# Optimization experiments

Hardware: AMD Instinct MI355X
Metric: run time of the kernel (lower is better)

Reference implementation:

```python
import jax, jax.numpy as jnp
import numpy as np

H = 16  # n_heads

def setup_inputs() -> dict:
    key = jax.random.key(0)
    ks = jax.random.split(key, 7)
    B, L, D = 4, 2048, 1024
    s = 0.02
    return {
        "z": jax.random.normal(ks[0], (B, L, D), jnp.float32),
        "connection": jax.random.normal(ks[1], (B, L, D), jnp.float32),
        "Wq": jax.random.normal(ks[2], (2 * D, D), jnp.float32) * s,
        "Wk": jax.random.normal(ks[3], (2 * D, D), jnp.float32) * s,
        "Wv": jax.random.normal(ks[4], (D, D), jnp.float32) * s,
        "Wo": jax.random.normal(ks[5], (D, D), jnp.float32) * s,
        "temp": jnp.float32(1.0),
    }

def reference(z, connection, Wq, Wk, Wv, Wo, temp):
    B, L, D = z.shape
    hd = D // H
    zc = jnp.concatenate([z, connection], axis=-1)          # [B,L,2D]
    Q = (zc @ Wq).reshape(B, L, H, hd).transpose(0, 2, 1, 3)  # [B,H,L,hd]
    K = (zc @ Wk).reshape(B, L, H, hd).transpose(0, 2, 1, 3)
    V = (z @ Wv).reshape(B, L, H, hd).transpose(0, 2, 1, 3)
    scale = (hd ** -0.5) * temp
    scores = jnp.einsum('bhqd,bhkd->bhqk', Q, K) * scale     # [B,H,L,L]
    rel = jax.nn.sigmoid(scores)
    rel_sum = jnp.clip(rel.sum(-1, keepdims=True), 1.0, None)
    out = jnp.einsum('bhqk,bhkd->bhqd', rel, V) / rel_sum
    out = out.transpose(0, 2, 1, 3).reshape(B, L, D)
    return out @ Wo
```

## Files before the change

kernel.cpp:

```cpp
#include <hip/hip_runtime.h>

typedef unsigned short u16;
typedef unsigned int u32;
typedef __bf16 bf16x8 __attribute__((ext_vector_type(8)));
typedef float f32x4 __attribute__((ext_vector_type(4)));

#define DEV static __device__ __forceinline__

DEV void gload16(const void* g, void* l) {
    __builtin_amdgcn_global_load_lds(
        (const __attribute__((address_space(1))) void*)g,
        (__attribute__((address_space(3))) void*)l, 16, 0, 0);
}

DEV void store_c(float* p, float v) { *p = v; }
DEV void store_c(u16* p, float v) { *(__bf16*)p = (__bf16)v; }

DEV int swz(int row, int bytecol) { return row * 128 + (bytecol ^ ((row & 7) << 4)); }
DEV int swzP(int row, int bytecol) {
    return row * 128 + (bytecol ^ ((row & 7) << 4) ^ (row & 8));
}

DEV void xcd_remap(int& bx, int& by, int gx, int gy) {
    int nwg = gx * gy;
    int bid = by * gx + bx;
    int logical = (bid & 7) * (nwg >> 3) + (bid >> 3);
    bx = logical % gx;
    by = logical / gx;
}

__global__ void pack_zc(const float* __restrict__ z, const float* __restrict__ cn,
                        u16* __restrict__ zc) {
    size_t i = ((size_t)blockIdx.x * blockDim.x + threadIdx.x) * 4;
    size_t t = i >> 11;
    int c = (int)(i & 2047);
    const float* src = (c < 1024) ? (z + t * 1024 + c) : (cn + t * 1024 + (c - 1024));
    float4 v = *reinterpret_cast<const float4*>(src);
    union { __bf16 h[4]; uint2 u; } o;
    o.h[0] = (__bf16)v.x; o.h[1] = (__bf16)v.y;
    o.h[2] = (__bf16)v.z; o.h[3] = (__bf16)v.w;
    *reinterpret_cast<uint2*>(zc + i) = o.u;
}

__global__ void transpose_conv_w(const float* __restrict__ W, u16* __restrict__ WT,
                                 int K, int N, const float* __restrict__ scl) {
    __shared__ float tile[32][33];
    float sc = scl ? scl[0] * 0.18033688011112042f : 1.0f;
    int n0 = blockIdx.x * 32, k0 = blockIdx.y * 32;
    int tx = threadIdx.x, ty = threadIdx.y;
    #pragma unroll
    for (int i = ty; i < 32; i += 8)
        tile[i][tx] = W[(size_t)(k0 + i) * N + n0 + tx];
    __syncthreads();
    #pragma unroll
    for (int i = ty; i < 32; i += 8)
        *(__bf16*)&WT[(size_t)(n0 + i) * K + k0 + tx] = (__bf16)(tile[tx][i] * sc);
}

__global__ void transpose_v(const u16* __restrict__ Vf, u16* __restrict__ Vt) {
    __shared__ u16 tile[32][33];
    int bh = blockIdx.z; int b = bh >> 4, h = bh & 15;
    int l0 = blockIdx.x * 32, d0 = blockIdx.y * 32;
    int tx = threadIdx.x, ty = threadIdx.y;
    #pragma unroll
    for (int i = ty; i < 32; i += 8)
        tile[i][tx] = Vf[(size_t)(b * 2048 + l0 + i) * 1024 + h * 64 + d0 + tx];
    __syncthreads();
    #pragma unroll
    for (int i = ty; i < 32; i += 8)
        Vt[((size_t)bh * 64 + d0 + i) * 2048 + l0 + tx] = tile[tx][i];
}

template <typename OutT>
__global__ __launch_bounds__(256, 2)
void gemm_bt(const u16* __restrict__ A, const u16* __restrict__ BT,
             OutT* __restrict__ C, int M, int N, int K,
             int lda, int ldb, int ldc) {
    __shared__ u16 As[128 * 64];
    __shared__ u16 Bs[128 * 64];
    const int tid = threadIdx.x;
    const int lane = tid & 63;
    const int wid = tid >> 6;
    int bx = blockIdx.x, by = blockIdx.y;
    xcd_remap(bx, by, gridDim.x, gridDim.y);
    const int m0 = bx * 128;
    const int n0 = by * 128;
    const int wr = (wid >> 1) * 64;
    const int wc = (wid & 1) * 64;

    f32x4 acc[4][4];
    #pragma unroll
    for (int i = 0; i < 4; ++i)
        #pragma unroll
        for (int j = 0; j < 4; ++j)
            acc[i][j] = f32x4{0.f, 0.f, 0.f, 0.f};

    const int srcoff = ((lane & 7) ^ (lane >> 3)) * 8;
    const int rb = wid * 32 + (lane >> 3);
    const u16* aptr[4]; const u16* bptr[4];
    #pragma unroll
    for (int p = 0; p < 4; ++p) {
        aptr[p] = A  + (size_t)(m0 + rb + p * 8) * lda + srcoff;
        bptr[p] = BT + (size_t)(n0 + rb + p * 8) * ldb + srcoff;
    }

    for (int k0 = 0; k0 < K; k0 += 64) {
        __syncthreads();
        #pragma unroll
        for (int p = 0; p < 4; ++p)
            gload16(aptr[p] + k0, (char*)As + (wid * 4 + p) * 1024);
        #pragma unroll
        for (int p = 0; p < 4; ++p)
            gload16(bptr[p] + k0, (char*)Bs + (wid * 4 + p) * 1024);
        __syncthreads();

        #pragma unroll
        for (int kk = 0; kk < 64; kk += 32) {
            bf16x8 af[4], bfr[4];
            #pragma unroll
            for (int i = 0; i < 4; ++i) {
                int row = wr + i * 16 + (lane & 15);
                af[i] = *reinterpret_cast<const bf16x8*>(
                    reinterpret_cast<const char*>(As) + swz(row, (kk + (lane >> 4) * 8) * 2));
            }
            #pragma unroll
            for (int j = 0; j < 4; ++j) {
                int row = wc + j * 16 + (lane & 15);
                bfr[j] = *reinterpret_cast<const bf16x8*>(
                    reinterpret_cast<const char*>(Bs) + swz(row, (kk + (lane >> 4) * 8) * 2));
            }
            #pragma unroll
            for (int i = 0; i < 4; ++i)
                #pragma unroll
                for (int j = 0; j < 4; ++j)
                    acc[i][j] = __builtin_amdgcn_mfma_f32_16x16x32_bf16(af[i], bfr[j], acc[i][j], 0, 0, 0);
        }
    }

    #pragma unroll
    for (int i = 0; i < 4; ++i)
        #pragma unroll
        for (int j = 0; j < 4; ++j)
            #pragma unroll
            for (int r = 0; r < 4; ++r) {
                int row = m0 + wr + i * 16 + (lane >> 4) * 4 + r;
                int col = n0 + wc + j * 16 + (lane & 15);
                store_c(&C[(size_t)row * ldc + col], acc[i][j][r]);
            }
}

__global__ __launch_bounds__(256, 2)
void attn_kernel(const u16* __restrict__ QKf, const u16* __restrict__ Vt,
                 u16* __restrict__ Oa) {
    constexpr int L = 2048, D = 1024, QKLD = 2048, HD = 64;
    __shared__ u16 Ks[2][64 * 64];
    __shared__ u16 Vs[2][64 * 64];
    __shared__ u16 Ps[4][32 * 64];

    const int tid = threadIdx.x;
    const int lane = tid & 63;
    const int wid = tid >> 6;
    const int hi = lane >> 4;
    const int lq = lane & 15;
    int bx = blockIdx.x, by = blockIdx.y;
    xcd_remap(bx, by, gridDim.x, gridDim.y);
    const int bh = by;
    const int b = bh >> 4, h = bh & 15;
    const int q0 = bx * 128;

    const u16* Qbase = QKf + (size_t)(b * L) * QKLD + h * HD;
    const u16* Kbase = Qbase + 1024;
    const u16* Vbase = Vt + (size_t)bh * HD * L;

    const int srcoff = ((lane & 7) ^ (lane >> 3)) * 8;
    const int rb = wid * 16 + (lane >> 3);
    const u16* kptr[2]; const u16* vptr[2];
    #pragma unroll
    for (int p = 0; p < 2; ++p) {
        kptr[p] = Kbase + (size_t)(rb + p * 8) * QKLD + srcoff;
        vptr[p] = Vbase + (size_t)(rb + p * 8) * L + srcoff;
    }

    bf16x8 qf[2][2];
    #pragma unroll
    for (int i = 0; i < 2; ++i)
        #pragma unroll
        for (int kx = 0; kx < 2; ++kx)
            qf[i][kx] = *reinterpret_cast<const bf16x8*>(
                Qbase + (size_t)(q0 + wid * 32 + i * 16 + lq) * QKLD + kx * 32 + hi * 8);

    #pragma unroll
    for (int p = 0; p < 2; ++p)
        gload16(kptr[p], (char*)Ks[0] + (wid * 2 + p) * 1024);
    #pragma unroll
    for (int p = 0; p < 2; ++p)
        gload16(vptr[p], (char*)Vs[0] + (wid * 2 + p) * 1024);

    bf16x8 onesf;
    #pragma unroll
    for (int j = 0; j < 8; ++j) onesf[j] = (__bf16)1.0f;

    f32x4 oacc[4][2];
    #pragma unroll
    for (int ct = 0; ct < 4; ++ct)
        #pragma unroll
        for (int i = 0; i < 2; ++i) oacc[ct][i] = f32x4{0.f, 0.f, 0.f, 0.f};
    f32x4 racc[2];
    racc[0] = f32x4{0.f, 0.f, 0.f, 0.f};
    racc[1] = f32x4{0.f, 0.f, 0.f, 0.f};

    __syncthreads();
    int cur = 0;

    for (int k0 = 0; k0 < L; k0 += 64) {
        if (k0 + 64 < L) {
            #pragma unroll
            for (int p = 0; p < 2; ++p)
                gload16(kptr[p] + (size_t)(k0 + 64) * QKLD, (char*)Ks[cur ^ 1] + (wid * 2 + p) * 1024);
            #pragma unroll
            for (int p = 0; p < 2; ++p)
                gload16(vptr[p] + (k0 + 64), (char*)Vs[cur ^ 1] + (wid * 2 + p) * 1024);
        }

        f32x4 s[4][2];
        #pragma unroll
        for (int ct = 0; ct < 4; ++ct)
            #pragma unroll
            for (int i = 0; i < 2; ++i) s[ct][i] = f32x4{0.f, 0.f, 0.f, 0.f};
        #pragma unroll
        for (int kx = 0; kx < 2; ++kx) {
            bf16x8 ak[4];
            #pragma unroll
            for (int ct = 0; ct < 4; ++ct) {
                int krow = ct * 16 + lq;
                ak[ct] = *reinterpret_cast<const bf16x8*>(
                    reinterpret_cast<const char*>(Ks[cur]) + swz(krow, kx * 64 + hi * 16));
            }
            #pragma unroll
            for (int ct = 0; ct < 4; ++ct)
                #pragma unroll
                for (int i = 0; i < 2; ++i)
                    s[ct][i] = __builtin_amdgcn_mfma_f32_16x16x32_bf16(ak[ct], qf[i][kx], s[ct][i], 0, 0, 0);
        }

        #pragma unroll
        for (int i = 0; i < 2; ++i) {
            int prow = i * 16 + lq;
            #pragma unroll
            for (int ct = 0; ct < 4; ++ct) {
                float t0 = 1.0f + __builtin_amdgcn_exp2f(-s[ct][i][0]);
                float t1 = 1.0f + __builtin_amdgcn_exp2f(-s[ct][i][1]);
                float t2 = 1.0f + __builtin_amdgcn_exp2f(-s[ct][i][2]);
                float t3 = 1.0f + __builtin_amdgcn_exp2f(-s[ct][i][3]);
                float m01 = t0 * t1, m23 = t2 * t3;
                float rall = __builtin_amdgcn_rcpf(m01 * m23);
                float r01 = m23 * rall, r23 = m01 * rall;
                union { __bf16 hh[4]; uint2 uu; } pk;
                pk.hh[0] = (__bf16)(t1 * r01);
                pk.hh[1] = (__bf16)(t0 * r01);
                pk.hh[2] = (__bf16)(t3 * r23);
                pk.hh[3] = (__bf16)(t2 * r23);
                *reinterpret_cast<uint2*>(reinterpret_cast<char*>(Ps[wid]) +
                    swzP(prow, ct * 32 + hi * 8)) = pk.uu;
            }
        }

        #pragma unroll
        for (int kx = 0; kx < 2; ++kx) {
            bf16x8 ap[2];
            #pragma unroll
            for (int i = 0; i < 2; ++i) {
                int prow = i * 16 + lq;
                union { u32 w[4]; bf16x8 v; } apu;
                *reinterpret_cast<uint2*>(&apu.w[0]) = *reinterpret_cast<const uint2*>(
                    reinterpret_cast<const char*>(Ps[wid]) + swzP(prow, kx * 64 + hi * 16));
                *reinterpret_cast<uint2*>(&apu.w[2]) = *reinterpret_cast<const uint2*>(
                    reinterpret_cast<const char*>(Ps[wid]) + swzP(prow, kx * 64 + hi * 16 + 8));
                ap[i] = apu.v;
            }
            racc[0] = __builtin_amdgcn_mfma_f32_16x16x32_bf16(ap[0], onesf, racc[0], 0, 0, 0);
            racc[1] = __builtin_amdgcn_mfma_f32_16x16x32_bf16(ap[1], onesf, racc[1], 0, 0, 0);
            #pragma unroll
            for (int ct = 0; ct < 4; ++ct) {
                int vrow = ct * 16 + lq;
                bf16x8 bv = *reinterpret_cast<const bf16x8*>(
                    reinterpret_cast<const char*>(Vs[cur]) + swz(vrow, kx * 64 + hi * 16));
                #pragma unroll
                for (int i = 0; i < 2; ++i)
                    oacc[ct][i] = __builtin_amdgcn_mfma_f32_16x16x32_bf16(ap[i], bv, oacc[ct][i], 0, 0, 0);
            }
        }

        __syncthreads();
        cur ^= 1;
    }

    float rdiv[2][4];
    #pragma unroll
    for (int i = 0; i < 2; ++i)
        #pragma unroll
        for (int r = 0; r < 4; ++r)
            rdiv[i][r] = __builtin_amdgcn_rcpf(fmaxf(racc[i][r], 1.0f));

    #pragma unroll
    for (int ct = 0; ct < 4; ++ct)
        #pragma unroll
        for (int i = 0; i < 2; ++i)
            #pragma unroll
            for (int r = 0; r < 4; ++r) {
                int row = q0 + wid * 32 + i * 16 + hi * 4 + r;
                int col = h * HD + ct * 16 + lq;
                *(__bf16*)&Oa[(size_t)(b * L + row) * D + col] =
                    (__bf16)(oacc[ct][i][r] * rdiv[i][r]);
            }
}

extern "C" void kernel_launch(void* const* d_in, const int* in_sizes, int n_in,
                              void* d_out, int out_size, void* d_ws, size_t ws_size,
                              hipStream_t stream) {
    const float* z    = (const float*)d_in[0];
    const float* cn   = (const float*)d_in[1];
    const float* Wq   = (const float*)d_in[2];
    const float* Wk   = (const float*)d_in[3];
    const float* Wv   = (const float*)d_in[4];
    const float* Wo   = (const float*)d_in[5];
    const float* temp = (const float*)d_in[6];

    char* ws = (char*)d_ws;
    u16* zc  = (u16*)ws; ws += (size_t)8192 * 2048 * 2;
    u16* WqT = (u16*)ws; ws += (size_t)1024 * 2048 * 2;
    u16* WkT = (u16*)ws; ws += (size_t)1024 * 2048 * 2;
    u16* WvT = (u16*)ws; ws += (size_t)1024 * 1024 * 2;
    u16* WoT = (u16*)ws; ws += (size_t)1024 * 1024 * 2;
    u16* QKf = (u16*)ws; ws += (size_t)8192 * 2048 * 2;
    u16* Vf  = (u16*)ws; ws += (size_t)8192 * 1024 * 2;
    u16* Vt  = zc;
    u16* Oa  = Vf;

    pack_zc<<<16384, 256, 0, stream>>>(z, cn, zc);

    dim3 tb(32, 8);
    transpose_conv_w<<<dim3(32, 64), tb, 0, stream>>>(Wq, WqT, 2048, 1024, temp);
    transpose_conv_w<<<dim3(32, 64), tb, 0, stream>>>(Wk, WkT, 2048, 1024, nullptr);
    transpose_conv_w<<<dim3(32, 32), tb, 0, stream>>>(Wv, WvT, 1024, 1024, nullptr);
    transpose_conv_w<<<dim3(32, 32), tb, 0, stream>>>(Wo, WoT, 1024, 1024, nullptr);

    gemm_bt<u16><<<dim3(64, 16), 256, 0, stream>>>(zc, WqT, QKf, 8192, 2048, 2048, 2048, 2048, 2048);
    gemm_bt<u16><<<dim3(64, 8),  256, 0, stream>>>(zc, WvT, Vf,  8192, 1024, 1024, 2048, 1024, 1024);

    transpose_v<<<dim3(64, 2, 64), tb, 0, stream>>>(Vf, Vt);

    attn_kernel<<<dim3(16, 64), 256, 0, stream>>>(QKf, Vt, Oa);

    gemm_bt<float><<<dim3(64, 8), 256, 0, stream>>>(Oa, WoT, (float*)d_out, 8192, 1024, 1024, 1024, 1024, 1024);
}
```

Baseline: 405.4 us.

## Add 256x256-tile 8-wave GEMM kernel for the fused QK projection

Introduces a new GEMM kernel with 512 threads computing 256x256 output tiles, double-buffered LDS loads, quadrant-wise MFMA with priority hints, and barriers between quadrants. It is used for the large combined Q/K projection in place of the 128x128 kernel, to raise arithmetic intensity and reduce global/L2 traffic per FLOP. LDS use grows to 128KB per block, so at most one block fits per CU despite the launch bounds, and the grid shrinks to 256 blocks, which may leave CUs underused.

```diff
diff --git a/kernel.cpp b/kernel.cpp
--- a/kernel.cpp
+++ b/kernel.cpp
@@ -149,6 +149,117 @@
             }
 }
 
+template <typename OutT>
+__global__ __launch_bounds__(512, 2)
+void gemm8_bt(const u16* __restrict__ A, const u16* __restrict__ BT,
+              OutT* __restrict__ C, int M, int N, int K,
+              int lda, int ldb, int ldc) {
+    __shared__ u16 As[2][256 * 64];
+    __shared__ u16 Bs[2][256 * 64];
+    const int tid = threadIdx.x;
+    const int lane = tid & 63;
+    const int wid = tid >> 6;
+    const int wm = wid >> 2;
+    const int wn = wid & 3;
+    const int hi = lane >> 4;
+    const int lq = lane & 15;
+    int bx = blockIdx.x, by = blockIdx.y;
+    xcd_remap(bx, by, gridDim.x, gridDim.y);
+    const int m0 = bx * 256;
+    const int n0 = by * 256;
+
+    f32x4 acc[8][4];
+    #pragma unroll
+    for (int i = 0; i < 8; ++i)
+        #pragma unroll
+        for (int j = 0; j < 4; ++j)
+            acc[i][j] = f32x4{0.f, 0.f, 0.f, 0.f};
+
+    const int srcoff = ((lane & 7) ^ (lane >> 3)) * 8;
+    const int rb = wid * 32 + (lane >> 3);
+    const u16* aptr[4]; const u16* bptr[4];
+    #pragma unroll
+    for (int p = 0; p < 4; ++p) {
+        aptr[p] = A  + (size_t)(m0 + rb + p * 8) * lda + srcoff;
+        bptr[p] = BT + (size_t)(n0 + rb + p * 8) * ldb + srcoff;
+    }
+
+    const int nt = K >> 6;
+
+    #pragma unroll
+    for (int p = 0; p < 4; ++p) gload16(aptr[p], (char*)As[0] + (wid * 4 + p) * 1024);
+    #pragma unroll
+    for (int p = 0; p < 4; ++p) gload16(bptr[p], (char*)Bs[0] + (wid * 4 + p) * 1024);
+    #pragma unroll
+    for (int p = 0; p < 4; ++p) gload16(aptr[p] + 64, (char*)As[1] + (wid * 4 + p) * 1024);
+    #pragma unroll
+    for (int p = 0; p < 4; ++p) gload16(bptr[p] + 64, (char*)Bs[1] + (wid * 4 + p) * 1024);
+    asm volatile("s_waitcnt vmcnt(8)" ::: "memory");
+    __builtin_amdgcn_s_barrier();
+    __builtin_amdgcn_sched_barrier(0);
+
+    int cur = 0;
+    for (int t = 0; t < nt; ++t) {
+        #pragma unroll
+        for (int q = 0; q < 4; ++q) {
+            const int mq = q >> 1, nq = q & 1;
+            bf16x8 af[4][2], bfr[2][2];
+            #pragma unroll
+            for (int kx = 0; kx < 2; ++kx) {
+                #pragma unroll
+                for (int mi = 0; mi < 4; ++mi) {
+                    int row = wm * 128 + mq * 64 + mi * 16 + lq;
+                    af[mi][kx] = *reinterpret_cast<const bf16x8*>(
+                        reinterpret_cast<const char*>(As[cur]) + swz(row, kx * 64 + hi * 16));
+                }
+                #pragma unroll
+                for (int ni = 0; ni < 2; ++ni) {
+                    int row = wn * 64 + nq * 32 + ni * 16 + lq;
+                    bfr[ni][kx] = *reinterpret_cast<const bf16x8*>(
+                        reinterpret_cast<const char*>(Bs[cur]) + swz(row, kx * 64 + hi * 16));
+                }
+            }
+            __builtin_amdgcn_s_setprio(1);
+            #pragma unroll
+            for (int kx = 0; kx < 2; ++kx)
+                #pragma unroll
+                for (int mi = 0; mi < 4; ++mi)
+                    #pragma unroll
+                    for (int ni = 0; ni < 2; ++ni)
+                        acc[mq * 4 + mi][nq * 2 + ni] = __builtin_amdgcn_mfma_f32_16x16x32_bf16(
+                            af[mi][kx], bfr[ni][kx], acc[mq * 4 + mi][nq * 2 + ni], 0, 0, 0);
+            __builtin_amdgcn_s_setprio(0);
+            __builtin_amdgcn_s_barrier();
+        }
+        __builtin_amdgcn_sched_barrier(0);
+        if (t + 2 < nt) {
+            const int k0n = (t + 2) * 64;
+            #pragma unroll
+            for (int p = 0; p < 4; ++p) gload16(aptr[p] + k0n, (char*)As[cur] + (wid * 4 + p) * 1024);
+            #pragma unroll
+            for (int p = 0; p < 4; ++p) gload16(bptr[p] + k0n, (char*)Bs[cur] + (wid * 4 + p) * 1024);
+            asm volatile("s_waitcnt vmcnt(8)" ::: "memory");
+            __builtin_amdgcn_s_barrier();
+        } else if (t + 1 < nt) {
+            asm volatile("s_waitcnt vmcnt(0)" ::: "memory");
+            __builtin_amdgcn_s_barrier();
+        }
+        __builtin_amdgcn_sched_barrier(0);
+        cur ^= 1;
+    }
+
+    #pragma unroll
+    for (int am = 0; am < 8; ++am)
+        #pragma unroll
+        for (int an = 0; an < 4; ++an)
+            #pragma unroll
+            for (int r = 0; r < 4; ++r) {
+                int row = m0 + wm * 128 + (am >> 2) * 64 + (am & 3) * 16 + hi * 4 + r;
+                int col = n0 + wn * 64 + (an >> 1) * 32 + (an & 1) * 16 + lq;
+                store_c(&C[(size_t)row * ldc + col], acc[am][an][r]);
+            }
+}
+
 __global__ __launch_bounds__(256, 2)
 void attn_kernel(const u16* __restrict__ QKf, const u16* __restrict__ Vt,
                  u16* __restrict__ Oa) {
@@ -345,8 +456,8 @@
     transpose_conv_w<<<dim3(32, 32), tb, 0, stream>>>(Wv, WvT, 1024, 1024, nullptr);
     transpose_conv_w<<<dim3(32, 32), tb, 0, stream>>>(Wo, WoT, 1024, 1024, nullptr);
 
-    gemm_bt<u16><<<dim3(64, 16), 256, 0, stream>>>(zc, WqT, QKf, 8192, 2048, 2048, 2048, 2048, 2048);
-    gemm_bt<u16><<<dim3(64, 8),  256, 0, stream>>>(zc, WvT, Vf,  8192, 1024, 1024, 2048, 1024, 1024);
+    gemm8_bt<u16><<<dim3(32, 8), 512, 0, stream>>>(zc, WqT, QKf, 8192, 2048, 2048, 2048, 2048, 2048);
+    gemm_bt<u16><<<dim3(64, 8), 256, 0, stream>>>(zc, WvT, Vf, 8192, 1024, 1024, 2048, 1024, 1024);
 
     transpose_v<<<dim3(64, 2, 64), tb, 0, stream>>>(Vf, Vt);
 
```

Result: faster. 395.9 us (-2.3%).
